# Kernel optimization log

Hardware: AMD Instinct MI355X
Metric: run time of the kernel (lower is better)

## Reference

```python
import jax, jax.numpy as jnp
import numpy as np

C = 256
C8 = C // 8

def setup_inputs() -> dict:
    key = jax.random.key(0)
    ks = jax.random.split(key, 7)
    B, H, W = 4, 64, 64
    x = jax.random.normal(ks[0], (B, C, H, W), dtype=jnp.float32)
    s = 1.0 / np.sqrt(C)
    Wq = jax.random.normal(ks[1], (C8, C), dtype=jnp.float32) * s
    bq = jnp.zeros((C8,), dtype=jnp.float32)
    Wk = jax.random.normal(ks[2], (C8, C), dtype=jnp.float32) * s
    bk = jnp.zeros((C8,), dtype=jnp.float32)
    Wv = jax.random.normal(ks[3], (C, C), dtype=jnp.float32) * s
    bv = jnp.zeros((C,), dtype=jnp.float32)
    return {"x": x, "Wq": Wq, "bq": bq, "Wk": Wk, "bk": bk, "Wv": Wv, "bv": bv}

def reference(x, Wq, bq, Wk, bk, Wv, bv):
    B, Cc, H, W = x.shape
    xf = x.reshape(B, Cc, H * W)                      # [B, C, N]
    # 1x1 convs == per-pixel linear projections
    q = jnp.einsum('dc,bcn->bdn', Wq, xf) + bq[None, :, None]   # [B, C/8, N]
    k = jnp.einsum('dc,bcn->bdn', Wk, xf) + bk[None, :, None]   # [B, C/8, N]
    v = jnp.einsum('dc,bcn->bdn', Wv, xf) + bv[None, :, None]   # [B, C,   N]
    scores = jnp.einsum('bdi,bdj->bij', q, k)         # [B, N, N] (no scaling, matching source)
    attn = jax.nn.softmax(scores, axis=-1)
    out = jnp.einsum('bcj,bij->bci', v, attn)         # [B, C, N]
    return out.reshape(B, Cc, H, W) + x
```

## Files before the change

### kernel.cpp

```cpp
#include <hip/hip_runtime.h>
#include <math.h>

#define CCH   256
#define NPIX  4096
#define BATCH 4

typedef __attribute__((ext_vector_type(8))) short s16x8;
typedef __attribute__((ext_vector_type(4))) float f32x4;

__device__ __forceinline__ unsigned short f2bf(float f) {
    unsigned int u = __float_as_uint(f);
    u += 0x7fff + ((u >> 16) & 1);
    return (unsigned short)(u >> 16);
}
__device__ __forceinline__ float bf2f(unsigned short h) {
    return __uint_as_float(((unsigned int)h) << 16);
}

__device__ __forceinline__ size_t qk_addr(int b, int n, int d) {
    return ((((size_t)b * 256 + (n >> 4)) * 64 + ((d >> 3) << 4) + (n & 15)) << 3) + (d & 7);
}
__device__ __forceinline__ size_t v_addr(int b, int j, int c) {
    return ((((((size_t)b * 64 + (j >> 6)) * 16 + (c >> 4)) * 2 + ((j >> 5) & 1)) * 64
            + (((j >> 3) & 3) << 4) + (c & 15)) << 3) + (j & 7);
}

__global__ __launch_bounds__(64) void wcast_kernel(
    const float* __restrict__ Wq, const float* __restrict__ bq,
    const float* __restrict__ Wk, const float* __restrict__ bk,
    const float* __restrict__ Wv, const float* __restrict__ bv,
    unsigned short* __restrict__ wfh, unsigned short* __restrict__ wfl,
    float* __restrict__ bias_ws)
{
    const int rt = blockIdx.x;
    const int lane = threadIdx.x, l15 = lane & 15, quad = lane >> 4;
    const float *Ws, *bs; int roff; float scale = 1.0f;
    if (rt < 2)      { Ws = Wq; bs = bq; roff = rt * 16;      scale = 1.44269504f; }
    else if (rt < 4) { Ws = Wk; bs = bk; roff = (rt - 2) * 16; }
    else             { Ws = Wv; bs = bv; roff = (rt - 4) * 16; }

    const float* wrow = Ws + (size_t)(roff + l15) * CCH + quad * 8;
    for (int kb = 0; kb < 8; ++kb) {
        s16x8 h, l;
        #pragma unroll
        for (int d = 0; d < 8; ++d) {
            float wv = wrow[kb * 32 + d] * scale;
            unsigned short hh = f2bf(wv);
            h[d] = (short)hh;
            l[d] = (short)f2bf(wv - bf2f(hh));
        }
        *(s16x8*)&wfh[(((size_t)rt * 8 + kb) * 64 + lane) * 8] = h;
        if (rt < 4) *(s16x8*)&wfl[(((size_t)rt * 8 + kb) * 64 + lane) * 8] = l;
    }
    if (lane < 16) bias_ws[rt * 16 + lane] = bs[roff + lane] * scale;
}

__global__ __launch_bounds__(256, 4) void proj_kernel(
    const float* __restrict__ x,
    const unsigned short* __restrict__ wfh, const unsigned short* __restrict__ wfl,
    const float* __restrict__ bias_ws,
    unsigned short* __restrict__ q_hi, unsigned short* __restrict__ q_lo,
    unsigned short* __restrict__ k_hi, unsigned short* __restrict__ k_lo,
    unsigned short* __restrict__ v_frag)
{
    const int t = threadIdx.x;
    const int rh = t >> 6, lane = t & 63, l15 = lane & 15, quad = lane >> 4;
    const int b = blockIdx.y;
    const int nt = blockIdx.x;

    const float* xb = x + (size_t)b * CCH * NPIX + nt * 16 + l15;
    s16x8 xh[8], xl[8];
    #pragma unroll
    for (int kb = 0; kb < 8; ++kb) {
        s16x8 vh, vl;
        #pragma unroll
        for (int d = 0; d < 8; ++d) {
            float xv = xb[(size_t)(kb * 32 + quad * 8 + d) * NPIX];
            unsigned short h = f2bf(xv);
            vh[d] = (short)h;
            vl[d] = (short)f2bf(xv - bf2f(h));
        }
        xh[kb] = vh; xl[kb] = vl;
    }

    const int n = nt * 16 + l15;
    #pragma unroll 1
    for (int tt = 0; tt < 5; ++tt) {
        const int rt = rh * 5 + tt;
        if (rt < 4) {
            f32x4 acc0 = {0.f, 0.f, 0.f, 0.f};
            f32x4 acc1 = {0.f, 0.f, 0.f, 0.f};
            #pragma unroll
            for (int kb = 0; kb < 8; ++kb) {
                s16x8 ah = *(const s16x8*)&wfh[(((size_t)rt * 8 + kb) * 64 + lane) * 8];
                s16x8 al = *(const s16x8*)&wfl[(((size_t)rt * 8 + kb) * 64 + lane) * 8];
                acc0 = __builtin_amdgcn_mfma_f32_16x16x32_bf16(ah, xh[kb], acc0, 0, 0, 0);
                acc1 = __builtin_amdgcn_mfma_f32_16x16x32_bf16(ah, xl[kb], acc1, 0, 0, 0);
                acc1 = __builtin_amdgcn_mfma_f32_16x16x32_bf16(al, xh[kb], acc1, 0, 0, 0);
            }
            #pragma unroll
            for (int rr = 0; rr < 4; ++rr) {
                const int rloc = quad * 4 + rr;
                const float val = acc0[rr] + acc1[rr] + bias_ws[rt * 16 + rloc];
                unsigned short h = f2bf(val);
                unsigned short l = f2bf(val - bf2f(h));
                if (rt < 2) {
                    const size_t a = qk_addr(b, n, rt * 16 + rloc);
                    q_hi[a] = h; q_lo[a] = l;
                } else {
                    const size_t a = qk_addr(b, n, (rt - 2) * 16 + rloc);
                    k_hi[a] = h; k_lo[a] = l;
                }
            }
        } else {
            f32x4 acc = {0.f, 0.f, 0.f, 0.f};
            #pragma unroll
            for (int kb = 0; kb < 8; ++kb) {
                s16x8 ah = *(const s16x8*)&wfh[(((size_t)rt * 8 + kb) * 64 + lane) * 8];
                acc = __builtin_amdgcn_mfma_f32_16x16x32_bf16(ah, xh[kb], acc, 0, 0, 0);
            }
            #pragma unroll
            for (int rr = 0; rr < 4; ++rr) {
                const int rloc = quad * 4 + rr;
                const float val = acc[rr] + bias_ws[rt * 16 + rloc];
                v_frag[v_addr(b, n, (rt - 4) * 16 + rloc)] = f2bf(val);
            }
        }
    }
}

#define BARRIER_LGKM() do { \
    asm volatile("s_waitcnt lgkmcnt(0)" ::: "memory"); \
    __builtin_amdgcn_s_barrier(); \
    asm volatile("" ::: "memory"); \
} while (0)

#define QK_STEP(KFH, KFL, BUFC) do { \
    f32x4 a0 = __builtin_amdgcn_mfma_f32_16x16x32_bf16((KFH), qfl0, (f32x4){0.f,0.f,0.f,0.f}, 0, 0, 0); \
    a0 = __builtin_amdgcn_mfma_f32_16x16x32_bf16((KFL), qfh0, a0, 0, 0, 0); \
    a0 = __builtin_amdgcn_mfma_f32_16x16x32_bf16((KFH), qfh0, a0, 0, 0, 0); \
    f32x4 a1 = __builtin_amdgcn_mfma_f32_16x16x32_bf16((KFH), qfl1, (f32x4){0.f,0.f,0.f,0.f}, 0, 0, 0); \
    a1 = __builtin_amdgcn_mfma_f32_16x16x32_bf16((KFL), qfh1, a1, 0, 0, 0); \
    a1 = __builtin_amdgcn_mfma_f32_16x16x32_bf16((KFH), qfh1, a1, 0, 0, 0); \
    unsigned int u0 = __float_as_uint(__builtin_exp2f(a0[0])) + 0x8000u; \
    unsigned int u1 = __float_as_uint(__builtin_exp2f(a0[1])) + 0x8000u; \
    unsigned int u2 = __float_as_uint(__builtin_exp2f(a0[2])) + 0x8000u; \
    unsigned int u3 = __float_as_uint(__builtin_exp2f(a0[3])) + 0x8000u; \
    uint2 pv0; \
    pv0.x = __builtin_amdgcn_perm(u1, u0, 0x07060302u); \
    pv0.y = __builtin_amdgcn_perm(u3, u2, 0x07060302u); \
    *(uint2*)&p_lds[jh][BUFC][0 * 2 + pfrag_jj][(prow * 16 + l15) * 8 + pcol] = pv0; \
    u0 = __float_as_uint(__builtin_exp2f(a1[0])) + 0x8000u; \
    u1 = __float_as_uint(__builtin_exp2f(a1[1])) + 0x8000u; \
    u2 = __float_as_uint(__builtin_exp2f(a1[2])) + 0x8000u; \
    u3 = __float_as_uint(__builtin_exp2f(a1[3])) + 0x8000u; \
    uint2 pv1; \
    pv1.x = __builtin_amdgcn_perm(u1, u0, 0x07060302u); \
    pv1.y = __builtin_amdgcn_perm(u3, u2, 0x07060302u); \
    *(uint2*)&p_lds[jh][BUFC][1 * 2 + pfrag_jj][(prow * 16 + l15) * 8 + pcol] = pv1; \
} while (0)

#define ATTN_BODY(T, BUFC, KU_H, KU_L, KL_H, KL_L, DO_QK) do { \
    const int jt = jh * 32 + (T); \
     \
    const s16x8 pf0 = *(const s16x8*)&p_lds[jh][BUFC][0][lane * 8]; \
    const s16x8 pf1 = *(const s16x8*)&p_lds[jh][BUFC][1][lane * 8]; \
    const s16x8 pf2 = *(const s16x8*)&p_lds[jh][BUFC][2][lane * 8]; \
    const s16x8 pf3 = *(const s16x8*)&p_lds[jh][BUFC][3][lane * 8]; \
     \
    const size_t vbase = (((size_t)jt * 16 + ch * 4) * 2) * 512; \
    const s16x8 v0 = *(const s16x8*)(vb + vbase); \
    const s16x8 v1 = *(const s16x8*)(vb + vbase + 512); \
    const s16x8 v2 = *(const s16x8*)(vb + vbase + 1024); \
    const s16x8 v3 = *(const s16x8*)(vb + vbase + 1536); \
    if (DO_QK) { QK_STEP(KU_H, KU_L, (BUFC) ^ 1); } \
     \
    { \
        const int tpp = ((T) + 2 < 32) ? (T) + 2 : 0; \
        const size_t koff = (size_t)((jh * 32 + tpp) * 4 + ch) * 512; \
        KL_H = *(const s16x8*)(khb + koff); \
        KL_L = *(const s16x8*)(klb + koff); \
    } \
     \
    if (ch == 0) { \
        lacc = __builtin_amdgcn_mfma_f32_16x16x32_bf16(ones, pf0, lacc, 0, 0, 0); \
        lacc = __builtin_amdgcn_mfma_f32_16x16x32_bf16(ones, pf1, lacc, 0, 0, 0); \
    } else if (ch == 1) { \
        lacc = __builtin_amdgcn_mfma_f32_16x16x32_bf16(ones, pf2, lacc, 0, 0, 0); \
        lacc = __builtin_amdgcn_mfma_f32_16x16x32_bf16(ones, pf3, lacc, 0, 0, 0); \
    } \
    BARRIER_LGKM(); \
     \
    const s16x8 v4 = *(const s16x8*)(vb + vbase + 2048); \
    const s16x8 v5 = *(const s16x8*)(vb + vbase + 2560); \
    const s16x8 v6 = *(const s16x8*)(vb + vbase + 3072); \
    const s16x8 v7 = *(const s16x8*)(vb + vbase + 3584); \
    __builtin_amdgcn_s_setprio(1); \
    acc[0] = __builtin_amdgcn_mfma_f32_16x16x32_bf16(v0, pf0, acc[0], 0, 0, 0); \
    acc[0] = __builtin_amdgcn_mfma_f32_16x16x32_bf16(v1, pf1, acc[0], 0, 0, 0); \
    acc[1] = __builtin_amdgcn_mfma_f32_16x16x32_bf16(v0, pf2, acc[1], 0, 0, 0); \
    acc[1] = __builtin_amdgcn_mfma_f32_16x16x32_bf16(v1, pf3, acc[1], 0, 0, 0); \
    acc[2] = __builtin_amdgcn_mfma_f32_16x16x32_bf16(v2, pf0, acc[2], 0, 0, 0); \
    acc[2] = __builtin_amdgcn_mfma_f32_16x16x32_bf16(v3, pf1, acc[2], 0, 0, 0); \
    acc[3] = __builtin_amdgcn_mfma_f32_16x16x32_bf16(v2, pf2, acc[3], 0, 0, 0); \
    acc[3] = __builtin_amdgcn_mfma_f32_16x16x32_bf16(v3, pf3, acc[3], 0, 0, 0); \
    acc[4] = __builtin_amdgcn_mfma_f32_16x16x32_bf16(v4, pf0, acc[4], 0, 0, 0); \
    acc[4] = __builtin_amdgcn_mfma_f32_16x16x32_bf16(v5, pf1, acc[4], 0, 0, 0); \
    acc[5] = __builtin_amdgcn_mfma_f32_16x16x32_bf16(v4, pf2, acc[5], 0, 0, 0); \
    acc[5] = __builtin_amdgcn_mfma_f32_16x16x32_bf16(v5, pf3, acc[5], 0, 0, 0); \
    acc[6] = __builtin_amdgcn_mfma_f32_16x16x32_bf16(v6, pf0, acc[6], 0, 0, 0); \
    acc[6] = __builtin_amdgcn_mfma_f32_16x16x32_bf16(v7, pf1, acc[6], 0, 0, 0); \
    acc[7] = __builtin_amdgcn_mfma_f32_16x16x32_bf16(v6, pf2, acc[7], 0, 0, 0); \
    acc[7] = __builtin_amdgcn_mfma_f32_16x16x32_bf16(v7, pf3, acc[7], 0, 0, 0); \
    __builtin_amdgcn_s_setprio(0); \
} while (0)

__global__ __launch_bounds__(512, 4) void attn_kernel(
    const unsigned short* __restrict__ q_hi, const unsigned short* __restrict__ q_lo,
    const unsigned short* __restrict__ k_hi, const unsigned short* __restrict__ k_lo,
    const unsigned short* __restrict__ v_frag,
    const float* __restrict__ x, float* __restrict__ out)
{
    __shared__ unsigned short p_lds[2][2][4][512];
    __shared__ f32x4 comb[2][4][4][64];
    __shared__ float lds_l[2][2][16];

    const int t = threadIdx.x;
    const int w = t >> 6, lane = t & 63, l15 = lane & 15, quad = lane >> 4;
    const int jh = w >> 2, ch = w & 3;

    const int f = blockIdx.x;
    const int xcd = f & 7;
    const int b = xcd >> 1;
    const int ib = ((xcd & 1) << 6) + (f >> 3);

    s16x8 qfh0, qfl0, qfh1, qfl1;
    {
        const size_t qo0 = ((size_t)b * 256 + ib * 2 + 0) * 512 + (size_t)lane * 8;
        const size_t qo1 = ((size_t)b * 256 + ib * 2 + 1) * 512 + (size_t)lane * 8;
        qfh0 = *(const s16x8*)(q_hi + qo0);  qfl0 = *(const s16x8*)(q_lo + qo0);
        qfh1 = *(const s16x8*)(q_hi + qo1);  qfl1 = *(const s16x8*)(q_lo + qo1);
    }

    const s16x8 ones = { (short)0x3F80, (short)0x3F80, (short)0x3F80, (short)0x3F80,
                         (short)0x3F80, (short)0x3F80, (short)0x3F80, (short)0x3F80 };

    f32x4 acc[8];
    #pragma unroll
    for (int i = 0; i < 8; ++i) acc[i] = (f32x4){0.f, 0.f, 0.f, 0.f};
    f32x4 lacc = {0.f, 0.f, 0.f, 0.f};

    const unsigned short* khb = k_hi + (size_t)b * 131072 + (size_t)lane * 8;
    const unsigned short* klb = k_lo + (size_t)b * 131072 + (size_t)lane * 8;
    const unsigned short* vb  = v_frag + (size_t)b * 1048576 + (size_t)lane * 8;

    const int prow = ((ch & 1) << 1) + (quad >> 1);
    const int pcol = ((quad & 1) << 2);
    const int pfrag_jj = ch >> 1;

    s16x8 ka_h, ka_l, kb_h, kb_l;
    {
        const size_t k0 = (size_t)((jh * 32 + 0) * 4 + ch) * 512;
        ka_h = *(const s16x8*)(khb + k0);
        ka_l = *(const s16x8*)(klb + k0);
    }
    QK_STEP(ka_h, ka_l, 0);
    {
        const size_t k1 = (size_t)((jh * 32 + 1) * 4 + ch) * 512;
        ka_h = *(const s16x8*)(khb + k1);
        ka_l = *(const s16x8*)(klb + k1);
    }
    BARRIER_LGKM();

    #pragma unroll 1
    for (int t2 = 0; t2 < 16; ++t2) {
        ATTN_BODY(2 * t2,     0, ka_h, ka_l, kb_h, kb_l, 1);
        ATTN_BODY(2 * t2 + 1, 1, kb_h, kb_l, ka_h, ka_l, (t2 < 15));
    }

    if (ch < 2 && lane < 16) lds_l[jh][ch][lane] = lacc[0];
    if (jh == 0) {
        #pragma unroll
        for (int ct = 0; ct < 4; ++ct)
            comb[0][ch][ct][lane] = acc[ct * 2 + 1];
    } else {
        #pragma unroll
        for (int ct = 0; ct < 4; ++ct)
            comb[1][ch][ct][lane] = acc[ct * 2 + 0];
    }
    __syncthreads();
    const float linv = 1.f / (lds_l[0][jh][l15] + lds_l[1][jh][l15]);
    const int ibase = (ib * 2 + jh) * 16 + l15;
    #pragma unroll
    for (int ct = 0; ct < 4; ++ct) {
        f32x4 a;
        if (jh == 0) a = acc[ct * 2 + 0];
        else         a = acc[ct * 2 + 1];
        a += comb[1 - jh][ch][ct][lane];
        #pragma unroll
        for (int rr = 0; rr < 4; ++rr) {
            const int c = ch * 64 + ct * 16 + quad * 4 + rr;
            const size_t idx = ((size_t)b * CCH + c) * NPIX + ibase;
            out[idx] = a[rr] * linv + x[idx];
        }
    }
}

extern "C" void kernel_launch(void* const* d_in, const int* in_sizes, int n_in,
                              void* d_out, int out_size, void* d_ws, size_t ws_size,
                              hipStream_t stream) {
    const float* x  = (const float*)d_in[0];
    const float* Wq = (const float*)d_in[1];
    const float* bq = (const float*)d_in[2];
    const float* Wk = (const float*)d_in[3];
    const float* bk = (const float*)d_in[4];
    const float* Wv = (const float*)d_in[5];
    const float* bv = (const float*)d_in[6];
    float* out = (float*)d_out;

    unsigned short* ws = (unsigned short*)d_ws;
    unsigned short* q_hi   = ws;
    unsigned short* q_lo   = ws + 524288;
    unsigned short* k_hi   = ws + 1048576;
    unsigned short* k_lo   = ws + 1572864;
    unsigned short* v_frag = ws + 2097152;
    unsigned short* wfh    = ws + 6291456;
    unsigned short* wfl    = ws + 6373376;
    float*          bias_ws = (float*)(ws + 6389760);

    wcast_kernel<<<20, 64, 0, stream>>>(Wq, bq, Wk, bk, Wv, bv, wfh, wfl, bias_ws);
    proj_kernel<<<dim3(256, BATCH), 256, 0, stream>>>(x, wfh, wfl, bias_ws,
                                                      q_hi, q_lo, k_hi, k_lo, v_frag);
    attn_kernel<<<512, 512, 0, stream>>>(q_hi, q_lo, k_hi, k_lo, v_frag, x, out);
}
```

Measured before the change: 163.3 us.

## Double query tile per block with 1024-thread blocks and unioned LDS

Each attention block now handles two query-row groups (ih) with 16 waves instead of 8, halving the grid to 256 blocks so the K/V streams loaded per block feed more queries. Shared memory for P tiles and the cross-half combine buffer is overlaid in a union, and the epilogue combine runs in two passes with extra barriers to fit the smaller buffer. The aim is fewer global K/V loads and better cache reuse. The cost is larger blocks, extra block-wide synchronisation, and possibly lower occupancy or fewer blocks than CUs.

After: 163.6 us. About the same (+0.2%).

```diff
diff --git a/kernel.cpp b/kernel.cpp
--- a/kernel.cpp
+++ b/kernel.cpp
@@ -149,7 +149,7 @@
     uint2 pv0; \
     pv0.x = __builtin_amdgcn_perm(u1, u0, 0x07060302u); \
     pv0.y = __builtin_amdgcn_perm(u3, u2, 0x07060302u); \
-    *(uint2*)&p_lds[jh][BUFC][0 * 2 + pfrag_jj][(prow * 16 + l15) * 8 + pcol] = pv0; \
+    *(uint2*)&shm.p[ih][jh][BUFC][0 * 2 + pfrag_jj][(prow * 16 + l15) * 8 + pcol] = pv0; \
     u0 = __float_as_uint(__builtin_exp2f(a1[0])) + 0x8000u; \
     u1 = __float_as_uint(__builtin_exp2f(a1[1])) + 0x8000u; \
     u2 = __float_as_uint(__builtin_exp2f(a1[2])) + 0x8000u; \
@@ -157,16 +157,16 @@
     uint2 pv1; \
     pv1.x = __builtin_amdgcn_perm(u1, u0, 0x07060302u); \
     pv1.y = __builtin_amdgcn_perm(u3, u2, 0x07060302u); \
-    *(uint2*)&p_lds[jh][BUFC][1 * 2 + pfrag_jj][(prow * 16 + l15) * 8 + pcol] = pv1; \
+    *(uint2*)&shm.p[ih][jh][BUFC][1 * 2 + pfrag_jj][(prow * 16 + l15) * 8 + pcol] = pv1; \
 } while (0)
 
 #define ATTN_BODY(T, BUFC, KU_H, KU_L, KL_H, KL_L, DO_QK) do { \
     const int jt = jh * 32 + (T); \
      \
-    const s16x8 pf0 = *(const s16x8*)&p_lds[jh][BUFC][0][lane * 8]; \
-    const s16x8 pf1 = *(const s16x8*)&p_lds[jh][BUFC][1][lane * 8]; \
-    const s16x8 pf2 = *(const s16x8*)&p_lds[jh][BUFC][2][lane * 8]; \
-    const s16x8 pf3 = *(const s16x8*)&p_lds[jh][BUFC][3][lane * 8]; \
+    const s16x8 pf0 = *(const s16x8*)&shm.p[ih][jh][BUFC][0][lane * 8]; \
+    const s16x8 pf1 = *(const s16x8*)&shm.p[ih][jh][BUFC][1][lane * 8]; \
+    const s16x8 pf2 = *(const s16x8*)&shm.p[ih][jh][BUFC][2][lane * 8]; \
+    const s16x8 pf3 = *(const s16x8*)&shm.p[ih][jh][BUFC][3][lane * 8]; \
      \
     const size_t vbase = (((size_t)jt * 16 + ch * 4) * 2) * 512; \
     const s16x8 v0 = *(const s16x8*)(vb + vbase); \
@@ -215,29 +215,34 @@
     __builtin_amdgcn_s_setprio(0); \
 } while (0)
 
-__global__ __launch_bounds__(512, 4) void attn_kernel(
+union AttnShMem {
+    unsigned short p[2][2][2][4][512];
+    f32x4 comb[2][2][4][2][64];
+};
+
+__global__ __launch_bounds__(1024, 4) void attn_kernel(
     const unsigned short* __restrict__ q_hi, const unsigned short* __restrict__ q_lo,
     const unsigned short* __restrict__ k_hi, const unsigned short* __restrict__ k_lo,
     const unsigned short* __restrict__ v_frag,
     const float* __restrict__ x, float* __restrict__ out)
 {
-    __shared__ unsigned short p_lds[2][2][4][512];
-    __shared__ f32x4 comb[2][4][4][64];
-    __shared__ float lds_l[2][2][16];
+    __shared__ AttnShMem shm;
+    __shared__ float lds_l[2][2][2][16];
 
     const int t = threadIdx.x;
     const int w = t >> 6, lane = t & 63, l15 = lane & 15, quad = lane >> 4;
-    const int jh = w >> 2, ch = w & 3;
+    const int ih = w >> 3, jh = (w >> 2) & 1, ch = w & 3;
 
     const int f = blockIdx.x;
     const int xcd = f & 7;
     const int b = xcd >> 1;
-    const int ib = ((xcd & 1) << 6) + (f >> 3);
+    const int ib = ((xcd & 1) << 5) + (f >> 3);
 
     s16x8 qfh0, qfl0, qfh1, qfl1;
     {
-        const size_t qo0 = ((size_t)b * 256 + ib * 2 + 0) * 512 + (size_t)lane * 8;
-        const size_t qo1 = ((size_t)b * 256 + ib * 2 + 1) * 512 + (size_t)lane * 8;
+        const int ti0 = ib * 4 + ih * 2;
+        const size_t qo0 = ((size_t)b * 256 + ti0 + 0) * 512 + (size_t)lane * 8;
+        const size_t qo1 = ((size_t)b * 256 + ti0 + 1) * 512 + (size_t)lane * 8;
         qfh0 = *(const s16x8*)(q_hi + qo0);  qfl0 = *(const s16x8*)(q_lo + qo0);
         qfh1 = *(const s16x8*)(q_hi + qo1);  qfl1 = *(const s16x8*)(q_lo + qo1);
     }
@@ -278,30 +283,44 @@
         ATTN_BODY(2 * t2 + 1, 1, kb_h, kb_l, ka_h, ka_l, (t2 < 15));
     }
 
-    if (ch < 2 && lane < 16) lds_l[jh][ch][lane] = lacc[0];
-    if (jh == 0) {
-        #pragma unroll
-        for (int ct = 0; ct < 4; ++ct)
-            comb[0][ch][ct][lane] = acc[ct * 2 + 1];
-    } else {
-        #pragma unroll
-        for (int ct = 0; ct < 4; ++ct)
-            comb[1][ch][ct][lane] = acc[ct * 2 + 0];
-    }
+    if (ch < 2 && lane < 16) lds_l[ih][jh][ch][lane] = lacc[0];
+    if (jh == 0) { shm.comb[ih][0][ch][0][lane] = acc[1]; shm.comb[ih][0][ch][1][lane] = acc[3]; }
+    else         { shm.comb[ih][1][ch][0][lane] = acc[0]; shm.comb[ih][1][ch][1][lane] = acc[2]; }
     __syncthreads();
-    const float linv = 1.f / (lds_l[0][jh][l15] + lds_l[1][jh][l15]);
-    const int ibase = (ib * 2 + jh) * 16 + l15;
-    #pragma unroll
-    for (int ct = 0; ct < 4; ++ct) {
-        f32x4 a;
-        if (jh == 0) a = acc[ct * 2 + 0];
-        else         a = acc[ct * 2 + 1];
-        a += comb[1 - jh][ch][ct][lane];
+    const float linv = 1.f / (lds_l[ih][0][jh][l15] + lds_l[ih][1][jh][l15]);
+    const int ibase = (ib * 4 + ih * 2 + jh) * 16 + l15;
+    {
+        f32x4 a0 = (jh == 0) ? acc[0] : acc[1];
+        f32x4 a1 = (jh == 0) ? acc[2] : acc[3];
+        a0 += shm.comb[ih][1 - jh][ch][0][lane];
+        a1 += shm.comb[ih][1 - jh][ch][1][lane];
         #pragma unroll
         for (int rr = 0; rr < 4; ++rr) {
-            const int c = ch * 64 + ct * 16 + quad * 4 + rr;
-            const size_t idx = ((size_t)b * CCH + c) * NPIX + ibase;
-            out[idx] = a[rr] * linv + x[idx];
+            const int c0 = ch * 64 + 0 * 16 + quad * 4 + rr;
+            const int c1 = ch * 64 + 1 * 16 + quad * 4 + rr;
+            const size_t i0 = ((size_t)b * CCH + c0) * NPIX + ibase;
+            const size_t i1 = ((size_t)b * CCH + c1) * NPIX + ibase;
+            out[i0] = a0[rr] * linv + x[i0];
+            out[i1] = a1[rr] * linv + x[i1];
+        }
+    }
+    __syncthreads();
+    if (jh == 0) { shm.comb[ih][0][ch][0][lane] = acc[5]; shm.comb[ih][0][ch][1][lane] = acc[7]; }
+    else         { shm.comb[ih][1][ch][0][lane] = acc[4]; shm.comb[ih][1][ch][1][lane] = acc[6]; }
+    __syncthreads();
+    {
+        f32x4 a2 = (jh == 0) ? acc[4] : acc[5];
+        f32x4 a3 = (jh == 0) ? acc[6] : acc[7];
+        a2 += shm.comb[ih][1 - jh][ch][0][lane];
+        a3 += shm.comb[ih][1 - jh][ch][1][lane];
+        #pragma unroll
+        for (int rr = 0; rr < 4; ++rr) {
+            const int c2 = ch * 64 + 2 * 16 + quad * 4 + rr;
+            const int c3 = ch * 64 + 3 * 16 + quad * 4 + rr;
+            const size_t i2 = ((size_t)b * CCH + c2) * NPIX + ibase;
+            const size_t i3 = ((size_t)b * CCH + c3) * NPIX + ibase;
+            out[i2] = a2[rr] * linv + x[i2];
+            out[i3] = a3[rr] * linv + x[i3];
         }
     }
 }
@@ -331,5 +350,5 @@
     wcast_kernel<<<20, 64, 0, stream>>>(Wq, bq, Wk, bk, Wv, bv, wfh, wfl, bias_ws);
     proj_kernel<<<dim3(256, BATCH), 256, 0, stream>>>(x, wfh, wfl, bias_ws,
                                                       q_hi, q_lo, k_hi, k_lo, v_frag);
-    attn_kernel<<<512, 512, 0, stream>>>(q_hi, q_lo, k_hi, k_lo, v_frag, x, out);
-}
+    attn_kernel<<<256, 1024, 0, stream>>>(q_hi, q_lo, k_hi, k_lo, v_frag, x, out);
+}
```

## Restructure projection kernel to stream x and balance Q/K/V tiles across waves

Applied to the files above, without the earlier changes.

The projection kernel no longer holds all eight hi/lo bf16 x fragments in registers. It now streams them one k-block at a time, accumulating each wave's one Q/K tile and four V tiles together in a single pass. Work is split evenly, one QK tile plus four V tiles per wave, instead of the old uneven 5-tile split where some waves skipped iterations. Q/K stores become 4-element vector stores instead of scalar stores. This lowers register pressure and load imbalance, but the projection is likely a small share of total time next to the attention kernel.

New measurement: 151.3 us. -7.3%, faster.

```diff
diff --git a/kernel.cpp b/kernel.cpp
--- a/kernel.cpp
+++ b/kernel.cpp
@@ -6,6 +6,7 @@
 #define BATCH 4
 
 typedef __attribute__((ext_vector_type(8))) short s16x8;
+typedef __attribute__((ext_vector_type(4))) short s16x4;
 typedef __attribute__((ext_vector_type(4))) float f32x4;
 
 __device__ __forceinline__ unsigned short f2bf(float f) {
@@ -69,62 +70,67 @@
     const int nt = blockIdx.x;
 
     const float* xb = x + (size_t)b * CCH * NPIX + nt * 16 + l15;
-    s16x8 xh[8], xl[8];
+
+    f32x4 aq0 = {0.f, 0.f, 0.f, 0.f};
+    f32x4 aq1 = {0.f, 0.f, 0.f, 0.f};
+    f32x4 av[4];
     #pragma unroll
+    for (int i = 0; i < 4; ++i) av[i] = (f32x4){0.f, 0.f, 0.f, 0.f};
+
+    #pragma unroll 2
     for (int kb = 0; kb < 8; ++kb) {
-        s16x8 vh, vl;
+        s16x8 xh, xl;
         #pragma unroll
         for (int d = 0; d < 8; ++d) {
             float xv = xb[(size_t)(kb * 32 + quad * 8 + d) * NPIX];
             unsigned short h = f2bf(xv);
-            vh[d] = (short)h;
-            vl[d] = (short)f2bf(xv - bf2f(h));
-        }
-        xh[kb] = vh; xl[kb] = vl;
+            xh[d] = (short)h;
+            xl[d] = (short)f2bf(xv - bf2f(h));
+        }
+        {
+            const s16x8 ah = *(const s16x8*)&wfh[(((size_t)rh * 8 + kb) * 64 + lane) * 8];
+            const s16x8 al = *(const s16x8*)&wfl[(((size_t)rh * 8 + kb) * 64 + lane) * 8];
+            aq0 = __builtin_amdgcn_mfma_f32_16x16x32_bf16(ah, xh, aq0, 0, 0, 0);
+            aq1 = __builtin_amdgcn_mfma_f32_16x16x32_bf16(ah, xl, aq1, 0, 0, 0);
+            aq1 = __builtin_amdgcn_mfma_f32_16x16x32_bf16(al, xh, aq1, 0, 0, 0);
+        }
+        #pragma unroll
+        for (int i = 0; i < 4; ++i) {
+            const int rt = 4 + rh * 4 + i;
+            const s16x8 ah = *(const s16x8*)&wfh[(((size_t)rt * 8 + kb) * 64 + lane) * 8];
+            av[i] = __builtin_amdgcn_mfma_f32_16x16x32_bf16(ah, xh, av[i], 0, 0, 0);
+        }
     }
 
     const int n = nt * 16 + l15;
-    #pragma unroll 1
-    for (int tt = 0; tt < 5; ++tt) {
-        const int rt = rh * 5 + tt;
-        if (rt < 4) {
-            f32x4 acc0 = {0.f, 0.f, 0.f, 0.f};
-            f32x4 acc1 = {0.f, 0.f, 0.f, 0.f};
-            #pragma unroll
-            for (int kb = 0; kb < 8; ++kb) {
-                s16x8 ah = *(const s16x8*)&wfh[(((size_t)rt * 8 + kb) * 64 + lane) * 8];
-                s16x8 al = *(const s16x8*)&wfl[(((size_t)rt * 8 + kb) * 64 + lane) * 8];
-                acc0 = __builtin_amdgcn_mfma_f32_16x16x32_bf16(ah, xh[kb], acc0, 0, 0, 0);
-                acc1 = __builtin_amdgcn_mfma_f32_16x16x32_bf16(ah, xl[kb], acc1, 0, 0, 0);
-                acc1 = __builtin_amdgcn_mfma_f32_16x16x32_bf16(al, xh[kb], acc1, 0, 0, 0);
-            }
-            #pragma unroll
-            for (int rr = 0; rr < 4; ++rr) {
-                const int rloc = quad * 4 + rr;
-                const float val = acc0[rr] + acc1[rr] + bias_ws[rt * 16 + rloc];
-                unsigned short h = f2bf(val);
-                unsigned short l = f2bf(val - bf2f(h));
-                if (rt < 2) {
-                    const size_t a = qk_addr(b, n, rt * 16 + rloc);
-                    q_hi[a] = h; q_lo[a] = l;
-                } else {
-                    const size_t a = qk_addr(b, n, (rt - 2) * 16 + rloc);
-                    k_hi[a] = h; k_lo[a] = l;
-                }
-            }
+    {
+        s16x4 h4, l4;
+        #pragma unroll
+        for (int rr = 0; rr < 4; ++rr) {
+            const int rloc = quad * 4 + rr;
+            const float val = aq0[rr] + aq1[rr] + bias_ws[rh * 16 + rloc];
+            const unsigned short h = f2bf(val);
+            h4[rr] = (short)h;
+            l4[rr] = (short)f2bf(val - bf2f(h));
+        }
+        if (rh < 2) {
+            const size_t a = qk_addr(b, n, rh * 16 + quad * 4);
+            *(s16x4*)&q_hi[a] = h4;
+            *(s16x4*)&q_lo[a] = l4;
         } else {
-            f32x4 acc = {0.f, 0.f, 0.f, 0.f};
-            #pragma unroll
-            for (int kb = 0; kb < 8; ++kb) {
-                s16x8 ah = *(const s16x8*)&wfh[(((size_t)rt * 8 + kb) * 64 + lane) * 8];
-                acc = __builtin_amdgcn_mfma_f32_16x16x32_bf16(ah, xh[kb], acc, 0, 0, 0);
-            }
-            #pragma unroll
-            for (int rr = 0; rr < 4; ++rr) {
-                const int rloc = quad * 4 + rr;
-                const float val = acc[rr] + bias_ws[rt * 16 + rloc];
-                v_frag[v_addr(b, n, (rt - 4) * 16 + rloc)] = f2bf(val);
-            }
+            const size_t a = qk_addr(b, n, (rh - 2) * 16 + quad * 4);
+            *(s16x4*)&k_hi[a] = h4;
+            *(s16x4*)&k_lo[a] = l4;
+        }
+    }
+    #pragma unroll
+    for (int i = 0; i < 4; ++i) {
+        const int vt = rh * 4 + i;
+        #pragma unroll
+        for (int rr = 0; rr < 4; ++rr) {
+            const int rloc = quad * 4 + rr;
+            const float val = av[i][rr] + bias_ws[(4 + vt) * 16 + rloc];
+            v_frag[v_addr(b, n, vt * 16 + rloc)] = f2bf(val);
         }
     }
 }
@@ -146,18 +152,18 @@
     unsigned int u1 = __float_as_uint(__builtin_exp2f(a0[1])) + 0x8000u; \
     unsigned int u2 = __float_as_uint(__builtin_exp2f(a0[2])) + 0x8000u; \
     unsigned int u3 = __float_as_uint(__builtin_exp2f(a0[3])) + 0x8000u; \
-    uint2 pv0; \
-    pv0.x = __builtin_amdgcn_perm(u1, u0, 0x07060302u); \
-    pv0.y = __builtin_amdgcn_perm(u3, u2, 0x07060302u); \
-    *(uint2*)&p_lds[jh][BUFC][0 * 2 + pfrag_jj][(prow * 16 + l15) * 8 + pcol] = pv0; \
+    uint2 pv; \
+    pv.x = __builtin_amdgcn_perm(u1, u0, 0x07060302u); \
+    pv.y = __builtin_amdgcn_perm(u3, u2, 0x07060302u); \
+    *(uint2*)&p_lds[jh][BUFC][0 * 2 + pfrag_jj][(prow * 16 + l15) * 8 + pcol] = pv; \
     u0 = __float_as_uint(__builtin_exp2f(a1[0])) + 0x8000u; \
     u1 = __float_as_uint(__builtin_exp2f(a1[1])) + 0x8000u; \
     u2 = __float_as_uint(__builtin_exp2f(a1[2])) + 0x8000u; \
     u3 = __float_as_uint(__builtin_exp2f(a1[3])) + 0x8000u; \
-    uint2 pv1; \
-    pv1.x = __builtin_amdgcn_perm(u1, u0, 0x07060302u); \
-    pv1.y = __builtin_amdgcn_perm(u3, u2, 0x07060302u); \
-    *(uint2*)&p_lds[jh][BUFC][1 * 2 + pfrag_jj][(prow * 16 + l15) * 8 + pcol] = pv1; \
+    uint2 pw; \
+    pw.x = __builtin_amdgcn_perm(u1, u0, 0x07060302u); \
+    pw.y = __builtin_amdgcn_perm(u3, u2, 0x07060302u); \
+    *(uint2*)&p_lds[jh][BUFC][1 * 2 + pfrag_jj][(prow * 16 + l15) * 8 + pcol] = pw; \
 } while (0)
 
 #define ATTN_BODY(T, BUFC, KU_H, KU_L, KL_H, KL_L, DO_QK) do { \
```
